# Kernel tuning notes

Measured on AMD Instinct MI355X. Metric: run time of the kernel, lower is better.

Reference implementation:

```python
import jax, jax.numpy as jnp
import numpy as np


def setup_inputs() -> dict:
    key = jax.random.key(0)
    k1, k2 = jax.random.split(key)
    L, B, H = 1024, 64, 1024
    encoder_outputs = jax.random.normal(k1, (L, B, H), dtype=jnp.float32)
    decoder_gru_out = jax.random.normal(k2, (1, B, H), dtype=jnp.float32)
    return {"encoder_outputs": encoder_outputs, "decoder_gru_out": decoder_gru_out}


def reference(encoder_outputs, decoder_gru_out):
    # scores[l,b] = sum_h enc[l,b,h] * dec[0,b,h]
    scores = jnp.einsum('lbh,bh->lb', encoder_outputs, decoder_gru_out[0])
    # softmax over the sequence (L) axis
    attn = jax.nn.softmax(scores, axis=0)  # [L, B]
    # context[b,h] = sum_l attn[l,b] * enc[l,b,h]
    context = jnp.einsum('lb,lbh->bh', attn, encoder_outputs)
    return context
```

## Files before the change

kernel.cpp:

```cpp
#include <hip/hip_runtime.h>
#include <math.h>

#define L_SEQ 1024
#define BATCH 64
#define HDIM  1024
#define WPB   4

__global__ __launch_bounds__(256) void attn_partial_kernel(
    const float* __restrict__ enc, const float* __restrict__ dec,
    float* __restrict__ wsC, float* __restrict__ wsML,
    int split, int chunk)
{
    const int tid  = threadIdx.x;
    const int lane = tid & 63;
    const int wave = tid >> 6;
    const int w    = blockIdx.x * WPB + wave;
    const int b    = w / split;
    const int k    = w - b * split;
    const int l0   = k * chunk;

    const float4* decv = (const float4*)(dec + (size_t)b * HDIM);
    const float4 d0 = decv[lane];
    const float4 d1 = decv[lane + 64];
    const float4 d2 = decv[lane + 128];
    const float4 d3 = decv[lane + 192];

    float m = -INFINITY;
    float lsum = 0.0f;
    float4 a0 = make_float4(0.f, 0.f, 0.f, 0.f);
    float4 a1 = a0, a2 = a0, a3 = a0;

    for (int l = l0; l < l0 + chunk; ++l) {
        const float4* row = (const float4*)(enc + ((size_t)l * BATCH + b) * HDIM);
        const float4 e0 = row[lane];
        const float4 e1 = row[lane + 64];
        const float4 e2 = row[lane + 128];
        const float4 e3 = row[lane + 192];

        float p = e0.x * d0.x + e0.y * d0.y + e0.z * d0.z + e0.w * d0.w;
        p += e1.x * d1.x + e1.y * d1.y + e1.z * d1.z + e1.w * d1.w;
        p += e2.x * d2.x + e2.y * d2.y + e2.z * d2.z + e2.w * d2.w;
        p += e3.x * d3.x + e3.y * d3.y + e3.z * d3.z + e3.w * d3.w;

        #pragma unroll
        for (int off = 32; off > 0; off >>= 1)
            p += __shfl_xor(p, off, 64);

        const float mn    = fmaxf(m, p);
        const float scale = __expf(m - mn);
        const float pe    = __expf(p - mn);
        m = mn;
        lsum = lsum * scale + pe;
        a0.x = a0.x * scale + pe * e0.x;  a0.y = a0.y * scale + pe * e0.y;
        a0.z = a0.z * scale + pe * e0.z;  a0.w = a0.w * scale + pe * e0.w;
        a1.x = a1.x * scale + pe * e1.x;  a1.y = a1.y * scale + pe * e1.y;
        a1.z = a1.z * scale + pe * e1.z;  a1.w = a1.w * scale + pe * e1.w;
        a2.x = a2.x * scale + pe * e2.x;  a2.y = a2.y * scale + pe * e2.y;
        a2.z = a2.z * scale + pe * e2.z;  a2.w = a2.w * scale + pe * e2.w;
        a3.x = a3.x * scale + pe * e3.x;  a3.y = a3.y * scale + pe * e3.y;
        a3.z = a3.z * scale + pe * e3.z;  a3.w = a3.w * scale + pe * e3.w;
    }

    const size_t r = (size_t)b * split + k;
    float4* C = (float4*)(wsC + r * (size_t)HDIM);
    C[lane]       = a0;
    C[lane + 64]  = a1;
    C[lane + 128] = a2;
    C[lane + 192] = a3;
    if (lane == 0) {
        wsML[2 * r]     = m;
        wsML[2 * r + 1] = lsum;
    }
}

__global__ __launch_bounds__(256) void attn_reduce_kernel(
    const float* __restrict__ wsC, const float* __restrict__ wsML,
    float* __restrict__ out, int split)
{
    const int b = blockIdx.x;
    const int t = threadIdx.x;

    float M = -INFINITY;
    for (int k = 0; k < split; ++k)
        M = fmaxf(M, wsML[2 * ((size_t)b * split + k)]);

    float Ltot = 0.0f;
    float4 acc = make_float4(0.f, 0.f, 0.f, 0.f);
    for (int k = 0; k < split; ++k) {
        const size_t r = (size_t)b * split + k;
        const float wgt = __expf(wsML[2 * r] - M);
        Ltot += wsML[2 * r + 1] * wgt;
        const float4 c = ((const float4*)(wsC + r * (size_t)HDIM))[t];
        acc.x += c.x * wgt;  acc.y += c.y * wgt;
        acc.z += c.z * wgt;  acc.w += c.w * wgt;
    }
    const float inv = 1.0f / Ltot;
    float4 o;
    o.x = acc.x * inv;  o.y = acc.y * inv;
    o.z = acc.z * inv;  o.w = acc.w * inv;
    ((float4*)(out + (size_t)b * HDIM))[t] = o;
}

extern "C" void kernel_launch(void* const* d_in, const int* in_sizes, int n_in,
                              void* d_out, int out_size, void* d_ws, size_t ws_size,
                              hipStream_t stream) {
    const float* enc = (const float*)d_in[0];
    const float* dec = (const float*)d_in[1];
    float* out = (float*)d_out;

    int split = 32;
    while (split > 1) {
        const size_t need = (size_t)BATCH * split * HDIM * sizeof(float)
                          + (size_t)BATCH * split * 2 * sizeof(float);
        if (need <= ws_size) break;
        split >>= 1;
    }
    const int chunk = L_SEQ / split;

    float* wsC  = (float*)d_ws;
    float* wsML = wsC + (size_t)BATCH * split * HDIM;

    const int nblocks = (BATCH * split) / WPB;
    attn_partial_kernel<<<nblocks, 256, 0, stream>>>(enc, dec, wsC, wsML, split, chunk);
    attn_reduce_kernel<<<BATCH, 256, 0, stream>>>(wsC, wsML, out, split);
}
```

Baseline: 368.1 us.

## Batch four sequence rows per online-softmax step and raise split factor

The partial kernel now loads four encoder rows per iteration, so more independent memory loads are in flight. It interleaves the four wave reductions and does one max/rescale per group of four rows instead of per row. The split rises from 32 to 64 chunks, doubling the number of waves, and the reduce kernel is spread over four times as many smaller blocks. In exchange it uses more registers per thread, with launch bounds asking for occupancy 4, and the workspace for partial results doubles in size, which adds reduce traffic.

New measurement: 385.5 us. 1.05x slower.

```diff
diff --git a/kernel.cpp b/kernel.cpp
--- a/kernel.cpp
+++ b/kernel.cpp
@@ -5,8 +5,17 @@
 #define BATCH 64
 #define HDIM  1024
 #define WPB   4
+#define NL    4
 
-__global__ __launch_bounds__(256) void attn_partial_kernel(
+static __device__ __forceinline__ float4 f4_scale(float4 a, float s) {
+    return make_float4(a.x * s, a.y * s, a.z * s, a.w * s);
+}
+static __device__ __forceinline__ float4 f4_fma(float4 acc, float s, float4 b) {
+    return make_float4(acc.x + s * b.x, acc.y + s * b.y,
+                       acc.z + s * b.z, acc.w + s * b.w);
+}
+
+__global__ __launch_bounds__(256, 4) void attn_partial_kernel(
     const float* __restrict__ enc, const float* __restrict__ dec,
     float* __restrict__ wsC, float* __restrict__ wsML,
     int split, int chunk)
@@ -20,65 +29,87 @@
     const int l0   = k * chunk;
 
     const float4* decv = (const float4*)(dec + (size_t)b * HDIM);
-    const float4 d0 = decv[lane];
-    const float4 d1 = decv[lane + 64];
-    const float4 d2 = decv[lane + 128];
-    const float4 d3 = decv[lane + 192];
+    float4 d[4];
+    #pragma unroll
+    for (int q = 0; q < 4; ++q) d[q] = decv[lane + 64 * q];
 
     float m = -INFINITY;
     float lsum = 0.0f;
-    float4 a0 = make_float4(0.f, 0.f, 0.f, 0.f);
-    float4 a1 = a0, a2 = a0, a3 = a0;
+    float4 acc[4];
+    #pragma unroll
+    for (int q = 0; q < 4; ++q) acc[q] = make_float4(0.f, 0.f, 0.f, 0.f);
 
-    for (int l = l0; l < l0 + chunk; ++l) {
-        const float4* row = (const float4*)(enc + ((size_t)l * BATCH + b) * HDIM);
-        const float4 e0 = row[lane];
-        const float4 e1 = row[lane + 64];
-        const float4 e2 = row[lane + 128];
-        const float4 e3 = row[lane + 192];
+    const float* base = enc + ((size_t)l0 * BATCH + b) * HDIM;
+    const size_t row_stride = (size_t)BATCH * HDIM;
 
-        float p = e0.x * d0.x + e0.y * d0.y + e0.z * d0.z + e0.w * d0.w;
-        p += e1.x * d1.x + e1.y * d1.y + e1.z * d1.z + e1.w * d1.w;
-        p += e2.x * d2.x + e2.y * d2.y + e2.z * d2.z + e2.w * d2.w;
-        p += e3.x * d3.x + e3.y * d3.y + e3.z * d3.z + e3.w * d3.w;
+    for (int l = 0; l < chunk; l += NL) {
+        float4 e[NL][4];
+        #pragma unroll
+        for (int r = 0; r < NL; ++r) {
+            const float4* row = (const float4*)(base + (size_t)r * row_stride);
+            #pragma unroll
+            for (int q = 0; q < 4; ++q) e[r][q] = row[lane + 64 * q];
+        }
+        base += (size_t)NL * row_stride;
+
+        float s[NL];
+        #pragma unroll
+        for (int r = 0; r < NL; ++r) {
+            float p = 0.f;
+            #pragma unroll
+            for (int q = 0; q < 4; ++q) {
+                p += e[r][q].x * d[q].x + e[r][q].y * d[q].y
+                   + e[r][q].z * d[q].z + e[r][q].w * d[q].w;
+            }
+            s[r] = p;
+        }
 
         #pragma unroll
-        for (int off = 32; off > 0; off >>= 1)
-            p += __shfl_xor(p, off, 64);
+        for (int off = 32; off > 0; off >>= 1) {
+            #pragma unroll
+            for (int r = 0; r < NL; ++r)
+                s[r] += __shfl_xor(s[r], off, 64);
+        }
 
-        const float mn    = fmaxf(m, p);
+        float mn = fmaxf(fmaxf(s[0], s[1]), fmaxf(s[2], s[3]));
+        mn = fmaxf(mn, m);
         const float scale = __expf(m - mn);
-        const float pe    = __expf(p - mn);
         m = mn;
-        lsum = lsum * scale + pe;
-        a0.x = a0.x * scale + pe * e0.x;  a0.y = a0.y * scale + pe * e0.y;
-        a0.z = a0.z * scale + pe * e0.z;  a0.w = a0.w * scale + pe * e0.w;
-        a1.x = a1.x * scale + pe * e1.x;  a1.y = a1.y * scale + pe * e1.y;
-        a1.z = a1.z * scale + pe * e1.z;  a1.w = a1.w * scale + pe * e1.w;
-        a2.x = a2.x * scale + pe * e2.x;  a2.y = a2.y * scale + pe * e2.y;
-        a2.z = a2.z * scale + pe * e2.z;  a2.w = a2.w * scale + pe * e2.w;
-        a3.x = a3.x * scale + pe * e3.x;  a3.y = a3.y * scale + pe * e3.y;
-        a3.z = a3.z * scale + pe * e3.z;  a3.w = a3.w * scale + pe * e3.w;
+        const float p0 = __expf(s[0] - mn);
+        const float p1 = __expf(s[1] - mn);
+        const float p2 = __expf(s[2] - mn);
+        const float p3 = __expf(s[3] - mn);
+        lsum = lsum * scale + (p0 + p1 + p2 + p3);
+
+        #pragma unroll
+        for (int q = 0; q < 4; ++q) {
+            float4 t = f4_scale(acc[q], scale);
+            t = f4_fma(t, p0, e[0][q]);
+            t = f4_fma(t, p1, e[1][q]);
+            t = f4_fma(t, p2, e[2][q]);
+            t = f4_fma(t, p3, e[3][q]);
+            acc[q] = t;
+        }
     }
 
     const size_t r = (size_t)b * split + k;
     float4* C = (float4*)(wsC + r * (size_t)HDIM);
-    C[lane]       = a0;
-    C[lane + 64]  = a1;
-    C[lane + 128] = a2;
-    C[lane + 192] = a3;
+    #pragma unroll
+    for (int q = 0; q < 4; ++q) C[lane + 64 * q] = acc[q];
     if (lane == 0) {
         wsML[2 * r]     = m;
         wsML[2 * r + 1] = lsum;
     }
 }
 
-__global__ __launch_bounds__(256) void attn_reduce_kernel(
+__global__ __launch_bounds__(64) void attn_reduce_kernel(
     const float* __restrict__ wsC, const float* __restrict__ wsML,
     float* __restrict__ out, int split)
 {
-    const int b = blockIdx.x;
-    const int t = threadIdx.x;
+    const int b  = blockIdx.x >> 2;
+    const int q  = blockIdx.x & 3;
+    const int t  = threadIdx.x;
+    const int f4 = q * 64 + t;
 
     float M = -INFINITY;
     for (int k = 0; k < split; ++k)
@@ -90,15 +121,13 @@
         const size_t r = (size_t)b * split + k;
         const float wgt = __expf(wsML[2 * r] - M);
         Ltot += wsML[2 * r + 1] * wgt;
-        const float4 c = ((const float4*)(wsC + r * (size_t)HDIM))[t];
+        const float4 c = ((const float4*)(wsC + r * (size_t)HDIM))[f4];
         acc.x += c.x * wgt;  acc.y += c.y * wgt;
         acc.z += c.z * wgt;  acc.w += c.w * wgt;
     }
     const float inv = 1.0f / Ltot;
-    float4 o;
-    o.x = acc.x * inv;  o.y = acc.y * inv;
-    o.z = acc.z * inv;  o.w = acc.w * inv;
-    ((float4*)(out + (size_t)b * HDIM))[t] = o;
+    ((float4*)(out + (size_t)b * HDIM))[f4] =
+        make_float4(acc.x * inv, acc.y * inv, acc.z * inv, acc.w * inv);
 }
 
 extern "C" void kernel_launch(void* const* d_in, const int* in_sizes, int n_in,
@@ -108,7 +137,7 @@
     const float* dec = (const float*)d_in[1];
     float* out = (float*)d_out;
 
-    int split = 32;
+    int split = 64;
     while (split > 1) {
         const size_t need = (size_t)BATCH * split * HDIM * sizeof(float)
                           + (size_t)BATCH * split * 2 * sizeof(float);
@@ -122,5 +151,5 @@
 
     const int nblocks = (BATCH * split) / WPB;
     attn_partial_kernel<<<nblocks, 256, 0, stream>>>(enc, dec, wsC, wsML, split, chunk);
-    attn_reduce_kernel<<<BATCH, 256, 0, stream>>>(wsC, wsML, out, split);
+    attn_reduce_kernel<<<BATCH * 4, 64, 0, stream>>>(wsC, wsML, out, split);
 }
```
